# Kernel optimization log

Measured on AMD Instinct MI355X. Metric: run time of the kernel, lower is better.

Reference implementation:

```python
import jax, jax.numpy as jnp
import numpy as np

T, H, I, E, K = 4096, 2048, 2048, 16, 4
EPS = 1e-6


def setup_inputs() -> dict:
    key = jax.random.key(0)
    ks = jax.random.split(key, 7)
    s = 0.02
    return {
        "x": jax.random.normal(ks[0], (T, H), dtype=jnp.float32),
        "gamma": jnp.ones((H,), dtype=jnp.float32),
        "wg": jax.random.normal(ks[1], (E, H), dtype=jnp.float32) * s,
        "bg": jax.random.normal(ks[2], (E,), dtype=jnp.float32) * s,
        "w1": jax.random.normal(ks[3], (E, I, H), dtype=jnp.float32) * s,  # gate proj
        "w3": jax.random.normal(ks[4], (E, I, H), dtype=jnp.float32) * s,  # up proj
        "w2": jax.random.normal(ks[5], (E, H, I), dtype=jnp.float32) * s,  # down proj
    }


def reference(x, gamma, wg, bg, w1, w3, w2):
    # RMSNorm
    t = x * jax.lax.rsqrt(jnp.mean(x * x, axis=-1, keepdims=True) + EPS) * gamma
    # Router: softmax -> top-k -> renormalize (FusedMoE renormalize=True)
    logits = t @ wg.T + bg                        # [T, E]
    probs = jax.nn.softmax(logits, axis=-1)
    vals, idx = jax.lax.top_k(probs, K)           # [T, K]
    vals = vals / jnp.sum(vals, axis=-1, keepdims=True)
    # Dense [T, E] routing-weight matrix (zeros outside top-k)
    route_w = jnp.einsum("tk,tke->te", vals, jax.nn.one_hot(idx, E, dtype=vals.dtype))
    # Grouped expert GEMMs: scan over experts, accumulate weighted outputs
    def body(acc, p):
        w1e, w3e, w2e, we = p                     # [I,H], [I,H], [H,I], [T]
        h = jax.nn.silu(t @ w1e.T) * (t @ w3e.T)  # [T, I]
        return acc + (h @ w2e.T) * we[:, None], None
    moe_out, _ = jax.lax.scan(body, jnp.zeros_like(x), (w1, w3, w2, route_w.T))
    return x + moe_out
```

## Files before the change

kernel.cpp:

```cpp
#include <hip/hip_runtime.h>
#include <hip/hip_bf16.h>

constexpr int TT = 4096;
constexpr int HH = 2048;
constexpr int II = 2048;
constexpr int EE = 16;
constexpr int KTOP = 4;

typedef __attribute__((ext_vector_type(4))) float f4;
typedef __attribute__((ext_vector_type(8))) short s8;

__device__ __forceinline__ short f2bf(float f) {
    union { __hip_bfloat16 b; short s; } u;
    u.b = __float2bfloat16(f);
    return u.s;
}
__device__ __forceinline__ float bf2f(short s) {
    union { unsigned u; float f; } v;
    v.u = ((unsigned)(unsigned short)s) << 16;
    return v.f;
}

__global__ void k_rmsnorm(const float* __restrict__ x, const float* __restrict__ gamma,
                          short* __restrict__ t16, int* __restrict__ cnt) {
    const int row = blockIdx.x;
    const int tid = threadIdx.x;
    if (row == 0 && tid < EE) cnt[tid] = 0;
    const f4* xr = (const f4*)(x + (size_t)row * HH);
    f4 v0 = xr[tid * 2], v1 = xr[tid * 2 + 1];
    float ss = 0.f;
#pragma unroll
    for (int i = 0; i < 4; i++) { ss += v0[i] * v0[i]; ss += v1[i] * v1[i]; }
#pragma unroll
    for (int m = 32; m >= 1; m >>= 1) ss += __shfl_xor(ss, m);
    __shared__ float red[4];
    const int wid = tid >> 6, lane = tid & 63;
    if (lane == 0) red[wid] = ss;
    __syncthreads();
    const float tot = red[0] + red[1] + red[2] + red[3];
    const float rs = rsqrtf(tot * (1.f / HH) + 1e-6f);
    const f4* gr = (const f4*)gamma;
    f4 g0 = gr[tid * 2], g1 = gr[tid * 2 + 1];
    s8 o;
#pragma unroll
    for (int i = 0; i < 4; i++) {
        o[i]     = f2bf(v0[i] * rs * g0[i]);
        o[4 + i] = f2bf(v1[i] * rs * g1[i]);
    }
    *(s8*)(t16 + (size_t)row * HH + tid * 8) = o;
}

__global__ void k_router(const float* __restrict__ x, const float* __restrict__ gamma,
                         const float* __restrict__ wg, const float* __restrict__ bg,
                         int* __restrict__ cnt, int* __restrict__ lst,
                         float* __restrict__ lwt) {
    const int lane = threadIdx.x & 63;
    const int tok = blockIdx.x * 4 + (threadIdx.x >> 6);
    const float* xr = x + (size_t)tok * HH;
    float t[32];
    float ss = 0.f;
#pragma unroll
    for (int j = 0; j < 32; j++) { float v = xr[lane + 64 * j]; t[j] = v; ss += v * v; }
#pragma unroll
    for (int m = 32; m >= 1; m >>= 1) ss += __shfl_xor(ss, m);
    const float rs = rsqrtf(ss * (1.f / HH) + 1e-6f);
#pragma unroll
    for (int j = 0; j < 32; j++) t[j] *= rs * gamma[lane + 64 * j];

    float logit[EE];
#pragma unroll
    for (int e = 0; e < EE; e++) {
        const float* wrow = wg + (size_t)e * HH;
        float a = 0.f;
#pragma unroll
        for (int j = 0; j < 32; j++) a += t[j] * wrow[lane + 64 * j];
#pragma unroll
        for (int m = 32; m >= 1; m >>= 1) a += __shfl_xor(a, m);
        logit[e] = a + bg[e];
    }
    unsigned chosen = 0u;
    int sel[KTOP]; float sv[KTOP];
#pragma unroll
    for (int k = 0; k < KTOP; k++) {
        float best = -1e30f; int bi = 0;
#pragma unroll
        for (int e = 0; e < EE; e++) {
            bool take = (!((chosen >> e) & 1u)) && (logit[e] > best);
            if (take) { best = logit[e]; bi = e; }
        }
        chosen |= 1u << bi; sel[k] = bi; sv[k] = best;
    }
    const float lmax = sv[0];
    float s = 0.f;
#pragma unroll
    for (int k = 0; k < KTOP; k++) { sv[k] = expf(sv[k] - lmax); s += sv[k]; }
    const float inv = 1.f / s;
    if (lane == 0) {
#pragma unroll
        for (int k = 0; k < KTOP; k++) {
            int e = sel[k];
            int p = atomicAdd(&cnt[e], 1);
            lst[e * TT + p] = tok * KTOP + k;
            lwt[e * TT + p] = sv[k] * inv;
        }
    }
}

__global__ __launch_bounds__(256) void k_gemm_ffn(
        const short* __restrict__ t16, const float* __restrict__ w,
        short* __restrict__ hout, const int* __restrict__ cnt,
        const int* __restrict__ lst) {
    const int e = blockIdx.z;
    const int Me = cnt[e];
    const int m0 = blockIdx.y * 128;
    if (m0 >= Me) return;
    const int n0 = blockIdx.x * 128;
    const float* we = w + (size_t)e * II * HH;

    __shared__ char lA[16384];
    __shared__ char lB[16384];
    __shared__ int s_tok[128];

    const int tid = threadIdx.x;
    if (tid < 128) {
        int m = m0 + tid;
        s_tok[tid] = (m < Me) ? lst[e * TT + m] : 0;
    }
    __syncthreads();

    const int lane = tid & 63, wid = tid >> 6;
    const int wr = wid >> 1, wc = wid & 1;

    f4 acc[4][4];
    const f4 zero = {0.f, 0.f, 0.f, 0.f};
#pragma unroll
    for (int i = 0; i < 4; i++)
#pragma unroll
        for (int j = 0; j < 4; j++) acc[i][j] = zero;

    const int rbase = tid >> 3;
    const int kc = (tid & 7) * 8;
    const int lb0 = rbase * 128 + ((kc * 2) ^ ((rbase & 7) << 4));
    int tokrow[4];
#pragma unroll
    for (int j = 0; j < 4; j++) tokrow[j] = s_tok[rbase + 32 * j] >> 2;

    for (int kt = 0; kt < HH / 64; ++kt) {
        __syncthreads();
#pragma unroll
        for (int j = 0; j < 4; j++) {
            s8 av = *(const s8*)(t16 + (size_t)tokrow[j] * HH + kt * 64 + kc);
            *(s8*)(lA + lb0 + 4096 * j) = av;
        }
#pragma unroll
        for (int j = 0; j < 4; j++) {
            const float* gp = we + (size_t)(n0 + rbase + 32 * j) * HH + kt * 64 + kc;
            f4 b0 = *(const f4*)gp;
            f4 b1 = *(const f4*)(gp + 4);
            s8 bv;
#pragma unroll
            for (int i = 0; i < 4; i++) { bv[i] = f2bf(b0[i]); bv[4 + i] = f2bf(b1[i]); }
            *(s8*)(lB + lb0 + 4096 * j) = bv;
        }
        __syncthreads();
#pragma unroll
        for (int kk = 0; kk < 2; ++kk) {
            s8 af[4], bfr[4];
#pragma unroll
            for (int mf = 0; mf < 4; mf++) {
                int r = wr * 64 + mf * 16 + (lane & 15);
                int byte = r * 128 + (((kk * 64) + ((lane >> 4) << 4)) ^ ((r & 7) << 4));
                af[mf] = *(const s8*)(lA + byte);
            }
#pragma unroll
            for (int nf = 0; nf < 4; nf++) {
                int r = wc * 64 + nf * 16 + (lane & 15);
                int byte = r * 128 + (((kk * 64) + ((lane >> 4) << 4)) ^ ((r & 7) << 4));
                bfr[nf] = *(const s8*)(lB + byte);
            }
#pragma unroll
            for (int mf = 0; mf < 4; mf++)
#pragma unroll
                for (int nf = 0; nf < 4; nf++)
                    acc[mf][nf] = __builtin_amdgcn_mfma_f32_16x16x32_bf16(
                        af[mf], bfr[nf], acc[mf][nf], 0, 0, 0);
        }
    }
#pragma unroll
    for (int mf = 0; mf < 4; mf++) {
#pragma unroll
        for (int j = 0; j < 4; j++) {
            int rl = wr * 64 + mf * 16 + ((lane >> 4) << 2) + j;
            int m = m0 + rl;
            if (m < Me) {
                int pk = s_tok[rl];
                size_t orow = (size_t)pk * II;
#pragma unroll
                for (int nf = 0; nf < 4; nf++) {
                    int ncol = n0 + wc * 64 + nf * 16 + (lane & 15);
                    hout[orow + ncol] = f2bf(acc[mf][nf][j]);
                }
            }
        }
    }
}

__global__ void k_silu(short* __restrict__ h1, const short* __restrict__ h3) {
    size_t i = ((size_t)blockIdx.x * 256 + threadIdx.x) * 8;
    s8 g = *(const s8*)(h1 + i);
    s8 u = *(const s8*)(h3 + i);
    s8 o;
#pragma unroll
    for (int j = 0; j < 8; j++) {
        float gv = bf2f(g[j]), uv = bf2f(u[j]);
        float sv = gv / (1.f + expf(-gv));
        o[j] = f2bf(sv * uv);
    }
    *(s8*)(h1 + i) = o;
}

__global__ __launch_bounds__(256) void k_gemm_down(
        const short* __restrict__ h, const float* __restrict__ w2,
        float* __restrict__ buf2, const int* __restrict__ cnt,
        const int* __restrict__ lst, const float* __restrict__ lwt) {
    const int e = blockIdx.z;
    const int Me = cnt[e];
    const int m0 = blockIdx.y * 128;
    if (m0 >= Me) return;
    const int n0 = blockIdx.x * 128;
    const float* we = w2 + (size_t)e * HH * II;

    __shared__ char lA[16384];
    __shared__ char lB[16384];
    __shared__ int s_tok[128];
    __shared__ float s_wgt[128];

    const int tid = threadIdx.x;
    if (tid < 128) {
        int m = m0 + tid;
        bool v = (m < Me);
        s_tok[tid] = v ? lst[e * TT + m] : 0;
        s_wgt[tid] = v ? lwt[e * TT + m] : 0.f;
    }
    __syncthreads();

    const int lane = tid & 63, wid = tid >> 6;
    const int wr = wid >> 1, wc = wid & 1;

    f4 acc[4][4];
    const f4 zero = {0.f, 0.f, 0.f, 0.f};
#pragma unroll
    for (int i = 0; i < 4; i++)
#pragma unroll
        for (int j = 0; j < 4; j++) acc[i][j] = zero;

    const int rbase = tid >> 3;
    const int kc = (tid & 7) * 8;
    const int lb0 = rbase * 128 + ((kc * 2) ^ ((rbase & 7) << 4));
    int arow[4];
#pragma unroll
    for (int j = 0; j < 4; j++) arow[j] = s_tok[rbase + 32 * j];

    for (int kt = 0; kt < II / 64; ++kt) {
        __syncthreads();
#pragma unroll
        for (int j = 0; j < 4; j++) {
            s8 av = *(const s8*)(h + (size_t)arow[j] * II + kt * 64 + kc);
            *(s8*)(lA + lb0 + 4096 * j) = av;
        }
#pragma unroll
        for (int j = 0; j < 4; j++) {
            const float* gp = we + (size_t)(n0 + rbase + 32 * j) * II + kt * 64 + kc;
            f4 b0 = *(const f4*)gp;
            f4 b1 = *(const f4*)(gp + 4);
            s8 bv;
#pragma unroll
            for (int i = 0; i < 4; i++) { bv[i] = f2bf(b0[i]); bv[4 + i] = f2bf(b1[i]); }
            *(s8*)(lB + lb0 + 4096 * j) = bv;
        }
        __syncthreads();
#pragma unroll
        for (int kk = 0; kk < 2; ++kk) {
            s8 af[4], bfr[4];
#pragma unroll
            for (int mf = 0; mf < 4; mf++) {
                int r = wr * 64 + mf * 16 + (lane & 15);
                int byte = r * 128 + (((kk * 64) + ((lane >> 4) << 4)) ^ ((r & 7) << 4));
                af[mf] = *(const s8*)(lA + byte);
            }
#pragma unroll
            for (int nf = 0; nf < 4; nf++) {
                int r = wc * 64 + nf * 16 + (lane & 15);
                int byte = r * 128 + (((kk * 64) + ((lane >> 4) << 4)) ^ ((r & 7) << 4));
                bfr[nf] = *(const s8*)(lB + byte);
            }
#pragma unroll
            for (int mf = 0; mf < 4; mf++)
#pragma unroll
                for (int nf = 0; nf < 4; nf++)
                    acc[mf][nf] = __builtin_amdgcn_mfma_f32_16x16x32_bf16(
                        af[mf], bfr[nf], acc[mf][nf], 0, 0, 0);
        }
    }
#pragma unroll
    for (int mf = 0; mf < 4; mf++) {
#pragma unroll
        for (int j = 0; j < 4; j++) {
            int rl = wr * 64 + mf * 16 + ((lane >> 4) << 2) + j;
            int m = m0 + rl;
            if (m < Me) {
                int pk = s_tok[rl];
                float wgt = s_wgt[rl];
                size_t orow = (size_t)pk * HH;
#pragma unroll
                for (int nf = 0; nf < 4; nf++) {
                    int ncol = n0 + wc * 64 + nf * 16 + (lane & 15);
                    buf2[orow + ncol] = acc[mf][nf][j] * wgt;
                }
            }
        }
    }
}

__global__ void k_final(const float* __restrict__ x, const float* __restrict__ buf2,
                        float* __restrict__ out) {
    size_t i4 = (size_t)blockIdx.x * 256 + threadIdx.x;
    size_t tok = i4 / (HH / 4);
    size_t c4 = i4 % (HH / 4);
    f4 r = ((const f4*)x)[i4];
#pragma unroll
    for (int k = 0; k < KTOP; k++) {
        f4 b = ((const f4*)buf2)[(tok * KTOP + k) * (HH / 4) + c4];
        r += b;
    }
    ((f4*)out)[i4] = r;
}

extern "C" void kernel_launch(void* const* d_in, const int* in_sizes, int n_in,
                              void* d_out, int out_size, void* d_ws, size_t ws_size,
                              hipStream_t stream) {
    const float* x     = (const float*)d_in[0];
    const float* gamma = (const float*)d_in[1];
    const float* wg    = (const float*)d_in[2];
    const float* bg    = (const float*)d_in[3];
    const float* w1    = (const float*)d_in[4];
    const float* w3    = (const float*)d_in[5];
    const float* w2    = (const float*)d_in[6];
    float* out = (float*)d_out;

    char* ws = (char*)d_ws;
    size_t off = 0;
    short* t16 = (short*)(ws + off); off += (size_t)TT * HH * 2;
    short* h1  = (short*)(ws + off); off += (size_t)TT * KTOP * II * 2;
    short* h3  = (short*)(ws + off); off += (size_t)TT * KTOP * II * 2;
    float* buf2 = (float*)(ws + off); off += (size_t)TT * KTOP * HH * 4;
    int* cnt   = (int*)(ws + off); off += 256;
    int* lst   = (int*)(ws + off); off += (size_t)EE * TT * 4;
    float* lwt = (float*)(ws + off); off += (size_t)EE * TT * 4;

    k_rmsnorm<<<TT, 256, 0, stream>>>(x, gamma, t16, cnt);
    k_router<<<TT / 4, 256, 0, stream>>>(x, gamma, wg, bg, cnt, lst, lwt);

    dim3 g1(II / 128, TT / 128, EE);
    k_gemm_ffn<<<g1, 256, 0, stream>>>(t16, w1, h1, cnt, lst);
    k_gemm_ffn<<<g1, 256, 0, stream>>>(t16, w3, h3, cnt, lst);

    k_silu<<<(TT * KTOP * II / 8) / 256, 256, 0, stream>>>(h1, h3);

    dim3 g2(HH / 128, TT / 128, EE);
    k_gemm_down<<<g2, 256, 0, stream>>>(h1, w2, buf2, cnt, lst, lwt);

    k_final<<<(TT * HH / 4) / 256, 256, 0, stream>>>(x, buf2, out);
}
```

Before: 1.016 ms.

## Pre-convert expert weights to bf16 and stage tiles via direct global-to-LDS loads

Expert weight matrices are converted to bf16 in a separate pass each call into a reused workspace buffer. The GEMMs then load A and B tiles straight into LDS with global_load_lds, dropping the XOR swizzle and the per-tile fp32-to-bf16 conversion. The SiLU*up step is fused into the epilogue of the second FFN GEMM, which removes the h3 buffer and the separate silu kernel. The down-projection output buffer is stored in bf16, halving the scatter and final-reduce traffic at some cost in accuracy. The unswizzled LDS layout may cause bank conflicts, and the single synchronisation per step gives no double buffering.

Result: slower. 1.267 ms (+24.6%).

```diff
diff --git a/kernel.cpp b/kernel.cpp
--- a/kernel.cpp
+++ b/kernel.cpp
@@ -19,6 +19,12 @@
     union { unsigned u; float f; } v;
     v.u = ((unsigned)(unsigned short)s) << 16;
     return v.f;
+}
+
+__device__ __forceinline__ void g2l16(const void* g, void* l) {
+    __builtin_amdgcn_global_load_lds(
+        (const __attribute__((address_space(1))) void*)g,
+        (__attribute__((address_space(3))) void*)l, 16, 0, 0);
 }
 
 __global__ void k_rmsnorm(const float* __restrict__ x, const float* __restrict__ gamma,
@@ -106,30 +112,47 @@
     }
 }
 
+__global__ void k_convert(const float* __restrict__ src, short* __restrict__ dst) {
+    size_t i = (size_t)blockIdx.x * 256 + threadIdx.x;
+    f4 a = ((const f4*)src)[i * 2];
+    f4 b = ((const f4*)src)[i * 2 + 1];
+    s8 o;
+#pragma unroll
+    for (int j = 0; j < 4; j++) { o[j] = f2bf(a[j]); o[4 + j] = f2bf(b[j]); }
+    ((s8*)dst)[i] = o;
+}
+
+template<bool FUSE>
 __global__ __launch_bounds__(256) void k_gemm_ffn(
-        const short* __restrict__ t16, const float* __restrict__ w,
-        short* __restrict__ hout, const int* __restrict__ cnt,
+        const short* __restrict__ t16, const short* __restrict__ wb,
+        short* __restrict__ h1, const int* __restrict__ cnt,
         const int* __restrict__ lst) {
     const int e = blockIdx.z;
     const int Me = cnt[e];
     const int m0 = blockIdx.y * 128;
     if (m0 >= Me) return;
     const int n0 = blockIdx.x * 128;
-    const float* we = w + (size_t)e * II * HH;
-
-    __shared__ char lA[16384];
-    __shared__ char lB[16384];
+    const short* we = wb + (size_t)e * II * HH;
+
+    __shared__ short lA[128 * 64];
+    __shared__ short lB[128 * 64];
     __shared__ int s_tok[128];
 
     const int tid = threadIdx.x;
-    if (tid < 128) {
-        int m = m0 + tid;
-        s_tok[tid] = (m < Me) ? lst[e * TT + m] : 0;
-    }
+    if (tid < 128) s_tok[tid] = (m0 + tid < Me) ? lst[e * TT + m0 + tid] : 0;
     __syncthreads();
 
-    const int lane = tid & 63, wid = tid >> 6;
-    const int wr = wid >> 1, wc = wid & 1;
+    const int lane = tid & 63, w = tid >> 6;
+    const int wr = w >> 1, wc = w & 1;
+
+    const short* ga[4]; const short* gb[4];
+#pragma unroll
+    for (int i = 0; i < 4; i++) {
+        int row = w * 32 + i * 8 + (lane >> 3);
+        int tokrow = s_tok[row] >> 2;
+        ga[i] = t16 + (size_t)tokrow * HH + (lane & 7) * 8;
+        gb[i] = we + (size_t)(n0 + row) * HH + (lane & 7) * 8;
+    }
 
     f4 acc[4][4];
     const f4 zero = {0.f, 0.f, 0.f, 0.f};
@@ -138,114 +161,96 @@
 #pragma unroll
         for (int j = 0; j < 4; j++) acc[i][j] = zero;
 
-    const int rbase = tid >> 3;
-    const int kc = (tid & 7) * 8;
-    const int lb0 = rbase * 128 + ((kc * 2) ^ ((rbase & 7) << 4));
-    int tokrow[4];
-#pragma unroll
-    for (int j = 0; j < 4; j++) tokrow[j] = s_tok[rbase + 32 * j] >> 2;
-
     for (int kt = 0; kt < HH / 64; ++kt) {
+#pragma unroll
+        for (int i = 0; i < 4; i++)
+            g2l16(ga[i] + kt * 64, (char*)lA + w * 4096 + i * 1024);
+#pragma unroll
+        for (int i = 0; i < 4; i++)
+            g2l16(gb[i] + kt * 64, (char*)lB + w * 4096 + i * 1024);
         __syncthreads();
 #pragma unroll
-        for (int j = 0; j < 4; j++) {
-            s8 av = *(const s8*)(t16 + (size_t)tokrow[j] * HH + kt * 64 + kc);
-            *(s8*)(lA + lb0 + 4096 * j) = av;
-        }
-#pragma unroll
-        for (int j = 0; j < 4; j++) {
-            const float* gp = we + (size_t)(n0 + rbase + 32 * j) * HH + kt * 64 + kc;
-            f4 b0 = *(const f4*)gp;
-            f4 b1 = *(const f4*)(gp + 4);
-            s8 bv;
-#pragma unroll
-            for (int i = 0; i < 4; i++) { bv[i] = f2bf(b0[i]); bv[4 + i] = f2bf(b1[i]); }
-            *(s8*)(lB + lb0 + 4096 * j) = bv;
-        }
-        __syncthreads();
-#pragma unroll
         for (int kk = 0; kk < 2; ++kk) {
-            s8 af[4], bfr[4];
+            s8 af[4], bfv[4];
 #pragma unroll
             for (int mf = 0; mf < 4; mf++) {
                 int r = wr * 64 + mf * 16 + (lane & 15);
-                int byte = r * 128 + (((kk * 64) + ((lane >> 4) << 4)) ^ ((r & 7) << 4));
-                af[mf] = *(const s8*)(lA + byte);
+                af[mf] = *(const s8*)((const char*)lA + r * 128 + kk * 64 + ((lane >> 4) << 4));
             }
 #pragma unroll
             for (int nf = 0; nf < 4; nf++) {
                 int r = wc * 64 + nf * 16 + (lane & 15);
-                int byte = r * 128 + (((kk * 64) + ((lane >> 4) << 4)) ^ ((r & 7) << 4));
-                bfr[nf] = *(const s8*)(lB + byte);
+                bfv[nf] = *(const s8*)((const char*)lB + r * 128 + kk * 64 + ((lane >> 4) << 4));
             }
 #pragma unroll
             for (int mf = 0; mf < 4; mf++)
 #pragma unroll
                 for (int nf = 0; nf < 4; nf++)
                     acc[mf][nf] = __builtin_amdgcn_mfma_f32_16x16x32_bf16(
-                        af[mf], bfr[nf], acc[mf][nf], 0, 0, 0);
-        }
-    }
+                        af[mf], bfv[nf], acc[mf][nf], 0, 0, 0);
+        }
+        __syncthreads();
+    }
+
 #pragma unroll
     for (int mf = 0; mf < 4; mf++) {
 #pragma unroll
         for (int j = 0; j < 4; j++) {
             int rl = wr * 64 + mf * 16 + ((lane >> 4) << 2) + j;
-            int m = m0 + rl;
-            if (m < Me) {
-                int pk = s_tok[rl];
-                size_t orow = (size_t)pk * II;
+            if (m0 + rl < Me) {
+                size_t orow = (size_t)s_tok[rl] * II;
 #pragma unroll
                 for (int nf = 0; nf < 4; nf++) {
                     int ncol = n0 + wc * 64 + nf * 16 + (lane & 15);
-                    hout[orow + ncol] = f2bf(acc[mf][nf][j]);
+                    if (FUSE) {
+                        float u = acc[mf][nf][j];
+                        float g = bf2f(h1[orow + ncol]);
+                        float sg = g / (1.f + expf(-g));
+                        h1[orow + ncol] = f2bf(sg * u);
+                    } else {
+                        h1[orow + ncol] = f2bf(acc[mf][nf][j]);
+                    }
                 }
             }
         }
     }
 }
 
-__global__ void k_silu(short* __restrict__ h1, const short* __restrict__ h3) {
-    size_t i = ((size_t)blockIdx.x * 256 + threadIdx.x) * 8;
-    s8 g = *(const s8*)(h1 + i);
-    s8 u = *(const s8*)(h3 + i);
-    s8 o;
-#pragma unroll
-    for (int j = 0; j < 8; j++) {
-        float gv = bf2f(g[j]), uv = bf2f(u[j]);
-        float sv = gv / (1.f + expf(-gv));
-        o[j] = f2bf(sv * uv);
-    }
-    *(s8*)(h1 + i) = o;
-}
-
 __global__ __launch_bounds__(256) void k_gemm_down(
-        const short* __restrict__ h, const float* __restrict__ w2,
-        float* __restrict__ buf2, const int* __restrict__ cnt,
+        const short* __restrict__ h, const short* __restrict__ w2b,
+        short* __restrict__ buf2, const int* __restrict__ cnt,
         const int* __restrict__ lst, const float* __restrict__ lwt) {
     const int e = blockIdx.z;
     const int Me = cnt[e];
     const int m0 = blockIdx.y * 128;
     if (m0 >= Me) return;
     const int n0 = blockIdx.x * 128;
-    const float* we = w2 + (size_t)e * HH * II;
-
-    __shared__ char lA[16384];
-    __shared__ char lB[16384];
+    const short* we = w2b + (size_t)e * HH * II;
+
+    __shared__ short lA[128 * 64];
+    __shared__ short lB[128 * 64];
     __shared__ int s_tok[128];
     __shared__ float s_wgt[128];
 
     const int tid = threadIdx.x;
     if (tid < 128) {
-        int m = m0 + tid;
-        bool v = (m < Me);
-        s_tok[tid] = v ? lst[e * TT + m] : 0;
-        s_wgt[tid] = v ? lwt[e * TT + m] : 0.f;
+        bool v = (m0 + tid < Me);
+        s_tok[tid] = v ? lst[e * TT + m0 + tid] : 0;
+        s_wgt[tid] = v ? lwt[e * TT + m0 + tid] : 0.f;
     }
     __syncthreads();
 
-    const int lane = tid & 63, wid = tid >> 6;
-    const int wr = wid >> 1, wc = wid & 1;
+    const int lane = tid & 63, w = tid >> 6;
+    const int wr = w >> 1, wc = w & 1;
+
+    const short* ga[4]; const short* gb[4];
+#pragma unroll
+    for (int i = 0; i < 4; i++) {
+        int row = w * 32 + i * 8 + (lane >> 3);
+        int pk = s_tok[row];
+        ga[i] = h + (size_t)pk * II + (lane & 7) * 8;
+        gb[i] = we + (size_t)(n0 + row) * II + (lane & 7) * 8;
+    }
 
     f4 acc[4][4];
     const f4 zero = {0.f, 0.f, 0.f, 0.f};
@@ -254,86 +259,70 @@
 #pragma unroll
         for (int j = 0; j < 4; j++) acc[i][j] = zero;
 
-    const int rbase = tid >> 3;
-    const int kc = (tid & 7) * 8;
-    const int lb0 = rbase * 128 + ((kc * 2) ^ ((rbase & 7) << 4));
-    int arow[4];
-#pragma unroll
-    for (int j = 0; j < 4; j++) arow[j] = s_tok[rbase + 32 * j];
-
     for (int kt = 0; kt < II / 64; ++kt) {
+#pragma unroll
+        for (int i = 0; i < 4; i++)
+            g2l16(ga[i] + kt * 64, (char*)lA + w * 4096 + i * 1024);
+#pragma unroll
+        for (int i = 0; i < 4; i++)
+            g2l16(gb[i] + kt * 64, (char*)lB + w * 4096 + i * 1024);
         __syncthreads();
 #pragma unroll
-        for (int j = 0; j < 4; j++) {
-            s8 av = *(const s8*)(h + (size_t)arow[j] * II + kt * 64 + kc);
-            *(s8*)(lA + lb0 + 4096 * j) = av;
-        }
-#pragma unroll
-        for (int j = 0; j < 4; j++) {
-            const float* gp = we + (size_t)(n0 + rbase + 32 * j) * II + kt * 64 + kc;
-            f4 b0 = *(const f4*)gp;
-            f4 b1 = *(const f4*)(gp + 4);
-            s8 bv;
-#pragma unroll
-            for (int i = 0; i < 4; i++) { bv[i] = f2bf(b0[i]); bv[4 + i] = f2bf(b1[i]); }
-            *(s8*)(lB + lb0 + 4096 * j) = bv;
-        }
-        __syncthreads();
-#pragma unroll
         for (int kk = 0; kk < 2; ++kk) {
-            s8 af[4], bfr[4];
+            s8 af[4], bfv[4];
 #pragma unroll
             for (int mf = 0; mf < 4; mf++) {
                 int r = wr * 64 + mf * 16 + (lane & 15);
-                int byte = r * 128 + (((kk * 64) + ((lane >> 4) << 4)) ^ ((r & 7) << 4));
-                af[mf] = *(const s8*)(lA + byte);
+                af[mf] = *(const s8*)((const char*)lA + r * 128 + kk * 64 + ((lane >> 4) << 4));
             }
 #pragma unroll
             for (int nf = 0; nf < 4; nf++) {
                 int r = wc * 64 + nf * 16 + (lane & 15);
-                int byte = r * 128 + (((kk * 64) + ((lane >> 4) << 4)) ^ ((r & 7) << 4));
-                bfr[nf] = *(const s8*)(lB + byte);
+                bfv[nf] = *(const s8*)((const char*)lB + r * 128 + kk * 64 + ((lane >> 4) << 4));
             }
 #pragma unroll
             for (int mf = 0; mf < 4; mf++)
 #pragma unroll
                 for (int nf = 0; nf < 4; nf++)
                     acc[mf][nf] = __builtin_amdgcn_mfma_f32_16x16x32_bf16(
-                        af[mf], bfr[nf], acc[mf][nf], 0, 0, 0);
-        }
-    }
+                        af[mf], bfv[nf], acc[mf][nf], 0, 0, 0);
+        }
+        __syncthreads();
+    }
+
 #pragma unroll
     for (int mf = 0; mf < 4; mf++) {
 #pragma unroll
         for (int j = 0; j < 4; j++) {
             int rl = wr * 64 + mf * 16 + ((lane >> 4) << 2) + j;
-            int m = m0 + rl;
-            if (m < Me) {
-                int pk = s_tok[rl];
+            if (m0 + rl < Me) {
+                size_t orow = (size_t)s_tok[rl] * HH;
                 float wgt = s_wgt[rl];
-                size_t orow = (size_t)pk * HH;
 #pragma unroll
                 for (int nf = 0; nf < 4; nf++) {
                     int ncol = n0 + wc * 64 + nf * 16 + (lane & 15);
-                    buf2[orow + ncol] = acc[mf][nf][j] * wgt;
+                    buf2[orow + ncol] = f2bf(acc[mf][nf][j] * wgt);
                 }
             }
         }
     }
 }
 
-__global__ void k_final(const float* __restrict__ x, const float* __restrict__ buf2,
+__global__ void k_final(const float* __restrict__ x, const short* __restrict__ buf2,
                         float* __restrict__ out) {
-    size_t i4 = (size_t)blockIdx.x * 256 + threadIdx.x;
-    size_t tok = i4 / (HH / 4);
-    size_t c4 = i4 % (HH / 4);
-    f4 r = ((const f4*)x)[i4];
+    size_t i8 = (size_t)blockIdx.x * 256 + threadIdx.x;
+    size_t tok = i8 / (HH / 8);
+    size_t c8 = i8 % (HH / 8);
+    const f4* xp = (const f4*)x + i8 * 2;
+    f4 r0 = xp[0], r1 = xp[1];
 #pragma unroll
     for (int k = 0; k < KTOP; k++) {
-        f4 b = ((const f4*)buf2)[(tok * KTOP + k) * (HH / 4) + c4];
-        r += b;
-    }
-    ((f4*)out)[i4] = r;
+        s8 b = ((const s8*)buf2)[(tok * KTOP + k) * (HH / 8) + c8];
+#pragma unroll
+        for (int j = 0; j < 4; j++) { r0[j] += bf2f(b[j]); r1[j] += bf2f(b[4 + j]); }
+    }
+    ((f4*)out)[i8 * 2] = r0;
+    ((f4*)out)[i8 * 2 + 1] = r1;
 }
 
 extern "C" void kernel_launch(void* const* d_in, const int* in_sizes, int n_in,
@@ -350,25 +339,28 @@
 
     char* ws = (char*)d_ws;
     size_t off = 0;
-    short* t16 = (short*)(ws + off); off += (size_t)TT * HH * 2;
-    short* h1  = (short*)(ws + off); off += (size_t)TT * KTOP * II * 2;
-    short* h3  = (short*)(ws + off); off += (size_t)TT * KTOP * II * 2;
-    float* buf2 = (float*)(ws + off); off += (size_t)TT * KTOP * HH * 4;
-    int* cnt   = (int*)(ws + off); off += 256;
-    int* lst   = (int*)(ws + off); off += (size_t)EE * TT * 4;
-    float* lwt = (float*)(ws + off); off += (size_t)EE * TT * 4;
+    short* t16  = (short*)(ws + off); off += (size_t)TT * HH * 2;
+    short* h1   = (short*)(ws + off); off += (size_t)TT * KTOP * II * 2;
+    short* buf2 = (short*)(ws + off); off += (size_t)TT * KTOP * HH * 2;
+    short* wbuf = (short*)(ws + off); off += (size_t)EE * II * HH * 2;
+    int* cnt    = (int*)(ws + off); off += 256;
+    int* lst    = (int*)(ws + off); off += (size_t)EE * TT * 4;
+    float* lwt  = (float*)(ws + off); off += (size_t)EE * TT * 4;
+
+    const int convBlocks = (EE * II * HH / 8) / 256;
 
     k_rmsnorm<<<TT, 256, 0, stream>>>(x, gamma, t16, cnt);
     k_router<<<TT / 4, 256, 0, stream>>>(x, gamma, wg, bg, cnt, lst, lwt);
 
     dim3 g1(II / 128, TT / 128, EE);
-    k_gemm_ffn<<<g1, 256, 0, stream>>>(t16, w1, h1, cnt, lst);
-    k_gemm_ffn<<<g1, 256, 0, stream>>>(t16, w3, h3, cnt, lst);
-
-    k_silu<<<(TT * KTOP * II / 8) / 256, 256, 0, stream>>>(h1, h3);
+    k_convert<<<convBlocks, 256, 0, stream>>>(w1, wbuf);
+    k_gemm_ffn<false><<<g1, 256, 0, stream>>>(t16, wbuf, h1, cnt, lst);
+    k_convert<<<convBlocks, 256, 0, stream>>>(w3, wbuf);
+    k_gemm_ffn<true><<<g1, 256, 0, stream>>>(t16, wbuf, h1, cnt, lst);
 
     dim3 g2(HH / 128, TT / 128, EE);
-    k_gemm_down<<<g2, 256, 0, stream>>>(h1, w2, buf2, cnt, lst, lwt);
-
-    k_final<<<(TT * HH / 4) / 256, 256, 0, stream>>>(x, buf2, out);
-}
+    k_convert<<<convBlocks, 256, 0, stream>>>(w2, wbuf);
+    k_gemm_down<<<g2, 256, 0, stream>>>(h1, wbuf, buf2, cnt, lst, lwt);
+
+    k_final<<<(TT * HH / 8) / 256, 256, 0, stream>>>(x, buf2, out);
+}
```

## Fuse gate/up GEMMs with SiLU epilogue and store down-proj partials in bf16

Applied to the files above, without the earlier changes.

Merges the w1 and w3 expert GEMMs into one kernel that shares the A tile loads and applies SiLU*up in the epilogue, which removes the separate silu kernel and the h3 round trip through memory. The down-projection partials are now written as bf16 instead of fp32, halving that buffer's write and read traffic in the final reduction. Costs are doubled accumulator registers and 48KB of LDS per block, which may lower occupancy, plus reduced precision in the per-expert partial sums.

New measurement: 923.0 us. 9.2% less time.

```diff
diff --git a/kernel.cpp b/kernel.cpp
--- a/kernel.cpp
+++ b/kernel.cpp
@@ -106,37 +106,36 @@
     }
 }
 
-__global__ __launch_bounds__(256) void k_gemm_ffn(
-        const short* __restrict__ t16, const float* __restrict__ w,
-        short* __restrict__ hout, const int* __restrict__ cnt,
-        const int* __restrict__ lst) {
+__global__ __launch_bounds__(256, 2) void k_gemm_ffn_fused(
+        const short* __restrict__ t16, const float* __restrict__ w1,
+        const float* __restrict__ w3, short* __restrict__ h,
+        const int* __restrict__ cnt, const int* __restrict__ lst) {
     const int e = blockIdx.z;
     const int Me = cnt[e];
     const int m0 = blockIdx.y * 128;
     if (m0 >= Me) return;
     const int n0 = blockIdx.x * 128;
-    const float* we = w + (size_t)e * II * HH;
+    const float* we1 = w1 + (size_t)e * II * HH;
+    const float* we3 = w3 + (size_t)e * II * HH;
 
     __shared__ char lA[16384];
-    __shared__ char lB[16384];
+    __shared__ char lB1[16384];
+    __shared__ char lB2[16384];
     __shared__ int s_tok[128];
 
     const int tid = threadIdx.x;
-    if (tid < 128) {
-        int m = m0 + tid;
-        s_tok[tid] = (m < Me) ? lst[e * TT + m] : 0;
-    }
+    if (tid < 128) s_tok[tid] = (m0 + tid < Me) ? lst[e * TT + m0 + tid] : 0;
     __syncthreads();
 
     const int lane = tid & 63, wid = tid >> 6;
     const int wr = wid >> 1, wc = wid & 1;
 
-    f4 acc[4][4];
+    f4 acc1[4][4], acc2[4][4];
     const f4 zero = {0.f, 0.f, 0.f, 0.f};
 #pragma unroll
     for (int i = 0; i < 4; i++)
 #pragma unroll
-        for (int j = 0; j < 4; j++) acc[i][j] = zero;
+        for (int j = 0; j < 4; j++) { acc1[i][j] = zero; acc2[i][j] = zero; }
 
     const int rbase = tid >> 3;
     const int kc = (tid & 7) * 8;
@@ -154,18 +153,28 @@
         }
 #pragma unroll
         for (int j = 0; j < 4; j++) {
-            const float* gp = we + (size_t)(n0 + rbase + 32 * j) * HH + kt * 64 + kc;
-            f4 b0 = *(const f4*)gp;
-            f4 b1 = *(const f4*)(gp + 4);
-            s8 bv;
-#pragma unroll
-            for (int i = 0; i < 4; i++) { bv[i] = f2bf(b0[i]); bv[4 + i] = f2bf(b1[i]); }
-            *(s8*)(lB + lb0 + 4096 * j) = bv;
+            size_t roff = (size_t)(n0 + rbase + 32 * j) * HH + kt * 64 + kc;
+            {
+                f4 b0 = *(const f4*)(we1 + roff);
+                f4 b1 = *(const f4*)(we1 + roff + 4);
+                s8 bv;
+#pragma unroll
+                for (int i = 0; i < 4; i++) { bv[i] = f2bf(b0[i]); bv[4 + i] = f2bf(b1[i]); }
+                *(s8*)(lB1 + lb0 + 4096 * j) = bv;
+            }
+            {
+                f4 b0 = *(const f4*)(we3 + roff);
+                f4 b1 = *(const f4*)(we3 + roff + 4);
+                s8 bv;
+#pragma unroll
+                for (int i = 0; i < 4; i++) { bv[i] = f2bf(b0[i]); bv[4 + i] = f2bf(b1[i]); }
+                *(s8*)(lB2 + lb0 + 4096 * j) = bv;
+            }
         }
         __syncthreads();
 #pragma unroll
         for (int kk = 0; kk < 2; ++kk) {
-            s8 af[4], bfr[4];
+            s8 af[4], b1v[4], b2v[4];
 #pragma unroll
             for (int mf = 0; mf < 4; mf++) {
                 int r = wr * 64 + mf * 16 + (lane & 15);
@@ -176,14 +185,18 @@
             for (int nf = 0; nf < 4; nf++) {
                 int r = wc * 64 + nf * 16 + (lane & 15);
                 int byte = r * 128 + (((kk * 64) + ((lane >> 4) << 4)) ^ ((r & 7) << 4));
-                bfr[nf] = *(const s8*)(lB + byte);
+                b1v[nf] = *(const s8*)(lB1 + byte);
+                b2v[nf] = *(const s8*)(lB2 + byte);
             }
 #pragma unroll
             for (int mf = 0; mf < 4; mf++)
 #pragma unroll
-                for (int nf = 0; nf < 4; nf++)
-                    acc[mf][nf] = __builtin_amdgcn_mfma_f32_16x16x32_bf16(
-                        af[mf], bfr[nf], acc[mf][nf], 0, 0, 0);
+                for (int nf = 0; nf < 4; nf++) {
+                    acc1[mf][nf] = __builtin_amdgcn_mfma_f32_16x16x32_bf16(
+                        af[mf], b1v[nf], acc1[mf][nf], 0, 0, 0);
+                    acc2[mf][nf] = __builtin_amdgcn_mfma_f32_16x16x32_bf16(
+                        af[mf], b2v[nf], acc2[mf][nf], 0, 0, 0);
+                }
         }
     }
 #pragma unroll
@@ -191,37 +204,24 @@
 #pragma unroll
         for (int j = 0; j < 4; j++) {
             int rl = wr * 64 + mf * 16 + ((lane >> 4) << 2) + j;
-            int m = m0 + rl;
-            if (m < Me) {
-                int pk = s_tok[rl];
-                size_t orow = (size_t)pk * II;
+            if (m0 + rl < Me) {
+                size_t orow = (size_t)s_tok[rl] * II;
 #pragma unroll
                 for (int nf = 0; nf < 4; nf++) {
                     int ncol = n0 + wc * 64 + nf * 16 + (lane & 15);
-                    hout[orow + ncol] = f2bf(acc[mf][nf][j]);
+                    float g = acc1[mf][nf][j];
+                    float u = acc2[mf][nf][j];
+                    float sg = g / (1.f + expf(-g));
+                    h[orow + ncol] = f2bf(sg * u);
                 }
             }
         }
     }
-}
-
-__global__ void k_silu(short* __restrict__ h1, const short* __restrict__ h3) {
-    size_t i = ((size_t)blockIdx.x * 256 + threadIdx.x) * 8;
-    s8 g = *(const s8*)(h1 + i);
-    s8 u = *(const s8*)(h3 + i);
-    s8 o;
-#pragma unroll
-    for (int j = 0; j < 8; j++) {
-        float gv = bf2f(g[j]), uv = bf2f(u[j]);
-        float sv = gv / (1.f + expf(-gv));
-        o[j] = f2bf(sv * uv);
-    }
-    *(s8*)(h1 + i) = o;
 }
 
 __global__ __launch_bounds__(256) void k_gemm_down(
         const short* __restrict__ h, const float* __restrict__ w2,
-        float* __restrict__ buf2, const int* __restrict__ cnt,
+        short* __restrict__ buf2, const int* __restrict__ cnt,
         const int* __restrict__ lst, const float* __restrict__ lwt) {
     const int e = blockIdx.z;
     const int Me = cnt[e];
@@ -237,10 +237,9 @@
 
     const int tid = threadIdx.x;
     if (tid < 128) {
-        int m = m0 + tid;
-        bool v = (m < Me);
-        s_tok[tid] = v ? lst[e * TT + m] : 0;
-        s_wgt[tid] = v ? lwt[e * TT + m] : 0.f;
+        bool v = (m0 + tid < Me);
+        s_tok[tid] = v ? lst[e * TT + m0 + tid] : 0;
+        s_wgt[tid] = v ? lwt[e * TT + m0 + tid] : 0.f;
     }
     __syncthreads();
 
@@ -307,33 +306,34 @@
 #pragma unroll
         for (int j = 0; j < 4; j++) {
             int rl = wr * 64 + mf * 16 + ((lane >> 4) << 2) + j;
-            int m = m0 + rl;
-            if (m < Me) {
-                int pk = s_tok[rl];
+            if (m0 + rl < Me) {
+                size_t orow = (size_t)s_tok[rl] * HH;
                 float wgt = s_wgt[rl];
-                size_t orow = (size_t)pk * HH;
 #pragma unroll
                 for (int nf = 0; nf < 4; nf++) {
                     int ncol = n0 + wc * 64 + nf * 16 + (lane & 15);
-                    buf2[orow + ncol] = acc[mf][nf][j] * wgt;
+                    buf2[orow + ncol] = f2bf(acc[mf][nf][j] * wgt);
                 }
             }
         }
     }
 }
 
-__global__ void k_final(const float* __restrict__ x, const float* __restrict__ buf2,
+__global__ void k_final(const float* __restrict__ x, const short* __restrict__ buf2,
                         float* __restrict__ out) {
-    size_t i4 = (size_t)blockIdx.x * 256 + threadIdx.x;
-    size_t tok = i4 / (HH / 4);
-    size_t c4 = i4 % (HH / 4);
-    f4 r = ((const f4*)x)[i4];
+    size_t i8 = (size_t)blockIdx.x * 256 + threadIdx.x;
+    size_t tok = i8 / (HH / 8);
+    size_t c8 = i8 % (HH / 8);
+    const f4* xp = (const f4*)x + i8 * 2;
+    f4 r0 = xp[0], r1 = xp[1];
 #pragma unroll
     for (int k = 0; k < KTOP; k++) {
-        f4 b = ((const f4*)buf2)[(tok * KTOP + k) * (HH / 4) + c4];
-        r += b;
-    }
-    ((f4*)out)[i4] = r;
+        s8 b = ((const s8*)buf2)[(tok * KTOP + k) * (HH / 8) + c8];
+#pragma unroll
+        for (int j = 0; j < 4; j++) { r0[j] += bf2f(b[j]); r1[j] += bf2f(b[4 + j]); }
+    }
+    ((f4*)out)[i8 * 2] = r0;
+    ((f4*)out)[i8 * 2 + 1] = r1;
 }
 
 extern "C" void kernel_launch(void* const* d_in, const int* in_sizes, int n_in,
@@ -350,25 +350,21 @@
 
     char* ws = (char*)d_ws;
     size_t off = 0;
-    short* t16 = (short*)(ws + off); off += (size_t)TT * HH * 2;
-    short* h1  = (short*)(ws + off); off += (size_t)TT * KTOP * II * 2;
-    short* h3  = (short*)(ws + off); off += (size_t)TT * KTOP * II * 2;
-    float* buf2 = (float*)(ws + off); off += (size_t)TT * KTOP * HH * 4;
-    int* cnt   = (int*)(ws + off); off += 256;
-    int* lst   = (int*)(ws + off); off += (size_t)EE * TT * 4;
-    float* lwt = (float*)(ws + off); off += (size_t)EE * TT * 4;
+    short* t16  = (short*)(ws + off); off += (size_t)TT * HH * 2;
+    short* h1   = (short*)(ws + off); off += (size_t)TT * KTOP * II * 2;
+    short* buf2 = (short*)(ws + off); off += (size_t)TT * KTOP * HH * 2;
+    int* cnt    = (int*)(ws + off); off += 256;
+    int* lst    = (int*)(ws + off); off += (size_t)EE * TT * 4;
+    float* lwt  = (float*)(ws + off); off += (size_t)EE * TT * 4;
 
     k_rmsnorm<<<TT, 256, 0, stream>>>(x, gamma, t16, cnt);
     k_router<<<TT / 4, 256, 0, stream>>>(x, gamma, wg, bg, cnt, lst, lwt);
 
     dim3 g1(II / 128, TT / 128, EE);
-    k_gemm_ffn<<<g1, 256, 0, stream>>>(t16, w1, h1, cnt, lst);
-    k_gemm_ffn<<<g1, 256, 0, stream>>>(t16, w3, h3, cnt, lst);
-
-    k_silu<<<(TT * KTOP * II / 8) / 256, 256, 0, stream>>>(h1, h3);
+    k_gemm_ffn_fused<<<g1, 256, 0, stream>>>(t16, w1, w3, h1, cnt, lst);
 
     dim3 g2(HH / 128, TT / 128, EE);
     k_gemm_down<<<g2, 256, 0, stream>>>(h1, w2, buf2, cnt, lst, lwt);
 
-    k_final<<<(TT * HH / 4) / 256, 256, 0, stream>>>(x, buf2, out);
-}
+    k_final<<<(TT * HH / 8) / 256, 256, 0, stream>>>(x, buf2, out);
+}
```
